# Performance work log

Hardware: AMD Instinct MI355X
Metric: run time of the kernel (lower is better)

## Reference

```python
import jax, jax.numpy as jnp
import numpy as np

B, S, D, H = 2, 2048, 1024, 16
HD = D // H  # head dim


def approx_gelu(x):
    return x * jax.nn.sigmoid(1.702 * x)


def setup_inputs() -> dict:
    key = jax.random.key(0)
    ks = jax.random.split(key, 12)
    q = jax.random.normal(ks[0], (B, S, D), jnp.float32)
    k = jax.random.normal(ks[1], (B, S, D), jnp.float32)
    v = jax.random.normal(ks[2], (B, S, D), jnp.float32)
    mask = jnp.zeros((B, 1, S, S), jnp.float32)
    sc = 0.02
    Wq = jax.random.normal(ks[3], (H, D, HD), jnp.float32) * sc
    bq = jax.random.normal(ks[4], (H, HD), jnp.float32) * sc
    Wk = jax.random.normal(ks[5], (H, D, HD), jnp.float32) * sc
    bk = jax.random.normal(ks[6], (H, HD), jnp.float32) * sc
    Wv = jax.random.normal(ks[7], (H, D, HD), jnp.float32) * sc
    bv = jax.random.normal(ks[8], (H, HD), jnp.float32) * sc
    Wo = jax.random.normal(ks[9], (D, D), jnp.float32) * sc
    bo = jax.random.normal(ks[10], (D,), jnp.float32) * sc
    return {"q": q, "k": k, "v": v, "mask": mask, "Wq": Wq, "bq": bq,
            "Wk": Wk, "bk": bk, "Wv": Wv, "bv": bv, "Wo": Wo, "bo": bo}


def reference(q, k, v, mask, Wq, bq, Wk, bk, Wv, bv, Wo, bo):
    # Per-head Q/K/V dense (no activation on projections, matching source).
    qh = jnp.einsum('bsd,hde->bhse', q, Wq) + bq[None, :, None, :]  # [B,H,S,HD]
    kh = jnp.einsum('bsd,hde->bhse', k, Wk) + bk[None, :, None, :]
    vh = jnp.einsum('bsd,hde->bhse', v, Wv) + bv[None, :, None, :]
    scale = 1.0 / jnp.sqrt(jnp.asarray(HD, qh.dtype))
    logits = jnp.einsum('bhse,bhte->bhst', qh, kh) * scale + mask  # [B,H,S,S]
    attn = jax.nn.softmax(logits, axis=-1)
    heads = jnp.einsum('bhst,bhte->bhse', attn, vh)  # [B,H,S,HD]
    # concat heads -> [B,S,D]
    x = jnp.transpose(heads, (0, 2, 1, 3)).reshape(q.shape[0], q.shape[1], D)
    return approx_gelu(x @ Wo + bo)
```

## Files before the change

### kernel.cpp

```cpp
#include <hip/hip_runtime.h>
#include <stdint.h>


typedef __bf16 bf16x8 __attribute__((ext_vector_type(8)));
typedef __bf16 bf16x4 __attribute__((ext_vector_type(4)));
typedef float f32x4 __attribute__((ext_vector_type(4)));
typedef float f32x16 __attribute__((ext_vector_type(16)));
typedef unsigned u32x4 __attribute__((ext_vector_type(4)));

static constexpr float L2E  = 1.4426950408889634f;
static constexpr float QSCL = 0.18033688011112042f;
static constexpr float GELC = -2.4554669595930157f;

__device__ __forceinline__ void async_load16(const void* g, void* l) {
    __builtin_amdgcn_global_load_lds(
        (const __attribute__((address_space(1))) unsigned int*)(uintptr_t)g,
        (__attribute__((address_space(3))) unsigned int*)(unsigned int)(uintptr_t)l,
        16, 0, 0);
}

template <int ROWS>
__device__ __forceinline__ void stage_tile(const __bf16* g, int ld, __bf16* lds, int tid) {
#pragma unroll
    for (int r = 0; r < ROWS / 32; ++r) {
        int p = r * 4096 + tid * 16;
        int row = p >> 7;
        int kbp = p & 127;
        int kbl = kbp ^ ((row & 7) << 4);
        async_load16((const char*)(g + (size_t)row * ld) + kbl,
                     (char*)lds + (p & ~1023));
    }
}

__device__ __forceinline__ bf16x8 lds_frag(const __bf16* base, int row, int kb) {
    return *(const bf16x8*)((const char*)base + (row << 7) + (kb ^ ((row & 7) << 4)));
}

__device__ __forceinline__ unsigned cvtpk(float a, float b) {
    unsigned d;
    asm("v_cvt_pk_bf16_f32 %0, %1, %2" : "=v"(d) : "v"(a), "v"(b));
    return d;
}
__device__ __forceinline__ void pswap(unsigned& a, unsigned& b) {
    asm("v_permlane32_swap_b32 %0, %1" : "+v"(a), "+v"(b));
}


__global__ __launch_bounds__(256) void cvt3_kernel(const float* __restrict__ q,
                                                   const float* __restrict__ k,
                                                   const float* __restrict__ v,
                                                   __bf16* __restrict__ qb,
                                                   __bf16* __restrict__ kb,
                                                   __bf16* __restrict__ vb) {
    int z = blockIdx.y;
    const float* src = z == 0 ? q : (z == 1 ? k : v);
    __bf16* dst = z == 0 ? qb : (z == 1 ? kb : vb);
    int i = blockIdx.x * 256 + threadIdx.x;
    f32x4 val = ((const f32x4*)src)[i];
    bf16x4 o;
    o[0] = (__bf16)val[0]; o[1] = (__bf16)val[1];
    o[2] = (__bf16)val[2]; o[3] = (__bf16)val[3];
    ((bf16x4*)dst)[i] = o;
}

__global__ __launch_bounds__(256) void flags_init(unsigned* __restrict__ flags) {
    int t = threadIdx.x;
#pragma unroll
    for (int k = 0; k < 4; ++k) flags[t + k * 256] = 0u;
}

__global__ __launch_bounds__(256) void mask_flags(const float* __restrict__ m,
                                                  unsigned* __restrict__ flags) {
    int i = blockIdx.x * 256 + threadIdx.x;
    f32x4 v = ((const f32x4*)m)[i];
    bool nz = (v[0] != 0.f) | (v[1] != 0.f) | (v[2] != 0.f) | (v[3] != 0.f);
    if (nz) {
        size_t i4 = (size_t)i * 4;
        int b = (int)(i4 >> 22);
        int rem = (int)(i4 & 4194303);
        int qq = rem >> 11, kv = rem & 2047;
        atomicOr(flags + (b * 16 + (qq >> 7)) * 32 + (kv >> 6), 1u);
    }
}

__global__ __launch_bounds__(256) void pack_wqkv(const float* __restrict__ Wq,
                                                 const float* __restrict__ Wk,
                                                 const float* __restrict__ Wv,
                                                 __bf16* __restrict__ out) {
    __shared__ __bf16 T[64][72];
    int tid = threadIdx.x;
    int k0 = blockIdx.x * 64, h = blockIdx.y, z = blockIdx.z;
    const float* W = z == 0 ? Wq : (z == 1 ? Wk : Wv);
#pragma unroll
    for (int it = 0; it < 4; ++it) {
        int idx = it * 1024 + tid * 4;
        int r = idx >> 6, e = idx & 63;
        f32x4 val = *(const f32x4*)(W + ((size_t)h * 1024 + k0 + r) * 64 + e);
#pragma unroll
        for (int j = 0; j < 4; ++j) T[r][e + j] = (__bf16)val[j];
    }
    __syncthreads();
    int e2 = tid >> 2, kc = (tid & 3) * 16;
    bf16x8 o0, o1;
#pragma unroll
    for (int i = 0; i < 8; ++i) { o0[i] = T[kc + i][e2]; o1[i] = T[kc + 8 + i][e2]; }
    __bf16* dst = out + ((size_t)z << 20) + (size_t)(h * 64 + e2) * 1024 + k0 + kc;
    *(bf16x8*)dst = o0;
    *(bf16x8*)(dst + 8) = o1;
}

__global__ __launch_bounds__(256) void pack_wo(const float* __restrict__ Wo,
                                               __bf16* __restrict__ out) {
    __shared__ __bf16 T[64][72];
    int tid = threadIdx.x;
    int k0 = blockIdx.x * 64, n0 = blockIdx.y * 64;
#pragma unroll
    for (int it = 0; it < 4; ++it) {
        int idx = it * 1024 + tid * 4;
        int r = idx >> 6, e = idx & 63;
        f32x4 val = *(const f32x4*)(Wo + (size_t)(k0 + r) * 1024 + n0 + e);
#pragma unroll
        for (int j = 0; j < 4; ++j) T[r][e + j] = (__bf16)val[j];
    }
    __syncthreads();
    int e2 = tid >> 2, kc = (tid & 3) * 16;
    bf16x8 o0, o1;
#pragma unroll
    for (int i = 0; i < 8; ++i) { o0[i] = T[kc + i][e2]; o1[i] = T[kc + 8 + i][e2]; }
    __bf16* dst = out + (size_t)(n0 + e2) * 1024 + k0 + kc;
    *(bf16x8*)dst = o0;
    *(bf16x8*)(dst + 8) = o1;
}

__global__ __launch_bounds__(256) void vtrans(const __bf16* __restrict__ vh,
                                              __bf16* __restrict__ vT) {
    __shared__ __bf16 T[64][72];
    int tid = threadIdx.x;
    int s0 = blockIdx.x * 64, bh = blockIdx.y, b = bh >> 4, h = bh & 15;
#pragma unroll
    for (int it = 0; it < 2; ++it) {
        int idx = it * 2048 + tid * 8;
        int r = idx >> 6, e0 = idx & 63;
        bf16x8 val = *(const bf16x8*)(vh + ((size_t)b * 2048 + s0 + r) * 1024 + h * 64 + e0);
#pragma unroll
        for (int j = 0; j < 8; ++j) T[r][e0 + j] = val[j];
    }
    __syncthreads();
    int e = tid >> 2, sc = (tid & 3) * 16;
    bf16x8 o0, o1;
#pragma unroll
    for (int i = 0; i < 8; ++i) { o0[i] = T[sc + i][e]; o1[i] = T[sc + 8 + i][e]; }
    __bf16* dst = vT + ((size_t)bh * 64 + e) * 2048 + s0 + sc;
    *(bf16x8*)dst = o0;
    *(bf16x8*)(dst + 8) = o1;
}

__global__ __launch_bounds__(256) void gemm_qkv(
    const __bf16* __restrict__ qb, const __bf16* __restrict__ kb,
    const __bf16* __restrict__ vb, const __bf16* __restrict__ w3,
    const float* __restrict__ bq, const float* __restrict__ bk,
    const float* __restrict__ bv,
    __bf16* __restrict__ qo, __bf16* __restrict__ ko, __bf16* __restrict__ vo) {
    __shared__ __bf16 As[128 * 64];
    __shared__ __bf16 Bs[128 * 64];
    int z = blockIdx.z;
    const __bf16* A = z == 0 ? qb : (z == 1 ? kb : vb);
    const __bf16* Bt = w3 + ((size_t)z << 20);
    const float* bias = z == 0 ? bq : (z == 1 ? bk : bv);
    __bf16* dst = z == 0 ? qo : (z == 1 ? ko : vo);
    float sc = z == 0 ? QSCL : 1.0f;

    int tid = threadIdx.x;
    int w = tid >> 6, lane = tid & 63, lg = lane >> 4, lr = lane & 15;
    int wr = (w >> 1) * 64, wc = (w & 1) * 64;
    int m0 = blockIdx.x * 128, n0 = blockIdx.y * 128;
    f32x4 acc[4][4] = {};
    for (int k0 = 0; k0 < 1024; k0 += 64) {
        __syncthreads();
        stage_tile<128>(A + (size_t)m0 * 1024 + k0, 1024, As, tid);
        stage_tile<128>(Bt + (size_t)n0 * 1024 + k0, 1024, Bs, tid);
        __syncthreads();
#pragma unroll
        for (int kk = 0; kk < 2; ++kk) {
            bf16x8 af[4], bfr[4];
#pragma unroll
            for (int t = 0; t < 4; ++t) {
                af[t] = lds_frag(As, wr + t * 16 + lr, lg * 16 + kk * 64);
                bfr[t] = lds_frag(Bs, wc + t * 16 + lr, lg * 16 + kk * 64);
            }
#pragma unroll
            for (int i = 0; i < 4; ++i)
#pragma unroll
                for (int j = 0; j < 4; ++j)
                    acc[i][j] = __builtin_amdgcn_mfma_f32_16x16x32_bf16(
                        af[i], bfr[j], acc[i][j], 0, 0, 0);
        }
    }
#pragma unroll
    for (int i = 0; i < 4; ++i) {
        int mb = m0 + wr + i * 16 + lg * 4;
#pragma unroll
        for (int j = 0; j < 4; ++j) {
            int n = n0 + wc + j * 16 + lr;
            float bvv = bias[n];
#pragma unroll
            for (int r = 0; r < 4; ++r)
                dst[(size_t)(mb + r) * 1024 + n] = (__bf16)((acc[i][j][r] + bvv) * sc);
        }
    }
}

__global__ __launch_bounds__(256) void gemm_out(const __bf16* __restrict__ A,
                                                const __bf16* __restrict__ Bt,
                                                const float* __restrict__ bias,
                                                float* __restrict__ dst) {
    __shared__ __bf16 As[64 * 64];
    __shared__ __bf16 Bs[128 * 64];
    int tid = threadIdx.x;
    int w = tid >> 6, lane = tid & 63, lg = lane >> 4, lr = lane & 15;
    int wr = (w >> 1) * 32, wc = (w & 1) * 64;
    int m0 = blockIdx.x * 64, n0 = blockIdx.y * 128;
    f32x4 acc[2][4] = {};
    for (int k0 = 0; k0 < 1024; k0 += 64) {
        __syncthreads();
        stage_tile<64>(A + (size_t)m0 * 1024 + k0, 1024, As, tid);
        stage_tile<128>(Bt + (size_t)n0 * 1024 + k0, 1024, Bs, tid);
        __syncthreads();
#pragma unroll
        for (int kk = 0; kk < 2; ++kk) {
            bf16x8 af[2], bfr[4];
#pragma unroll
            for (int t = 0; t < 2; ++t)
                af[t] = lds_frag(As, wr + t * 16 + lr, lg * 16 + kk * 64);
#pragma unroll
            for (int t = 0; t < 4; ++t)
                bfr[t] = lds_frag(Bs, wc + t * 16 + lr, lg * 16 + kk * 64);
#pragma unroll
            for (int i = 0; i < 2; ++i)
#pragma unroll
                for (int j = 0; j < 4; ++j)
                    acc[i][j] = __builtin_amdgcn_mfma_f32_16x16x32_bf16(
                        af[i], bfr[j], acc[i][j], 0, 0, 0);
        }
    }
#pragma unroll
    for (int i = 0; i < 2; ++i) {
        int mb = m0 + wr + i * 16 + lg * 4;
#pragma unroll
        for (int j = 0; j < 4; ++j) {
            int n = n0 + wc + j * 16 + lr;
            float bvv = bias[n];
#pragma unroll
            for (int r = 0; r < 4; ++r) {
                float v = acc[i][j][r] + bvv;
                float g = v / (1.f + exp2f(GELC * v));
                dst[(size_t)(mb + r) * 1024 + n] = g;
            }
        }
    }
}

__global__ __launch_bounds__(256) void attn_kernel(
    const __bf16* __restrict__ qs, const __bf16* __restrict__ ks,
    const __bf16* __restrict__ vT, const float* __restrict__ mask,
    const unsigned* __restrict__ flags,
    __bf16* __restrict__ Op0, __bf16* __restrict__ Op1,
    float* __restrict__ lacc) {
    __shared__ __bf16 Ks[2][64 * 64];
    __shared__ __bf16 Vs[2][64 * 64];
    int tid = threadIdx.x;
    int w = tid >> 6, l = tid & 63;
    int q31 = l & 31, hi = l >> 5;
    int i = blockIdx.x;
    int xcd = i & 7, j = i >> 3;
    int group = (j >> 4) * 8 + xcd;
    int qt = j & 15;
    int bh = group & 31, z = group >> 5;
    int b = bh >> 4, h = bh & 15;
    int qw = qt * 128 + w * 32;
    int kvbase = z << 10;

    const __bf16* Qp = qs + ((size_t)b * 2048 + qw + q31) * 1024 + h * 64 + hi * 8;
    bf16x8 qf[4];
#pragma unroll
    for (int kk = 0; kk < 4; ++kk) qf[kk] = *(const bf16x8*)(Qp + kk * 16);

    const __bf16* Kb = ks + ((size_t)b * 2048 + kvbase) * 1024 + h * 64;
    const __bf16* Vb = vT + (size_t)bh * 64 * 2048 + kvbase;
    const float* mrow = mask + (size_t)b * 4194304 + (size_t)(qw + q31) * 2048 + kvbase + hi * 4;
    const unsigned* flg = flags + (b * 16 + qt) * 32 + z * 16;

    f32x16 O[2] = {};
    float l_acc = 0.f;

    stage_tile<64>(Kb, 1024, Ks[0], tid);
    stage_tile<64>(Vb, 2048, Vs[0], tid);

    for (int kt = 0; kt < 16; ++kt) {
        int buf = kt & 1;
        __syncthreads();
        if (kt < 15) {
            stage_tile<64>(Kb + (size_t)(kt + 1) * 64 * 1024, 1024, Ks[buf ^ 1], tid);
            stage_tile<64>(Vb + (kt + 1) * 64, 2048, Vs[buf ^ 1], tid);
        }
        bf16x8 kf[2][4];
#pragma unroll
        for (int mt = 0; mt < 2; ++mt)
#pragma unroll
            for (int kk = 0; kk < 4; ++kk)
                kf[mt][kk] = lds_frag(Ks[buf], mt * 32 + q31, kk * 32 + hi * 16);
        f32x16 T[2] = {};
        __builtin_amdgcn_s_setprio(1);
#pragma unroll
        for (int kk = 0; kk < 4; ++kk)
#pragma unroll
            for (int mt = 0; mt < 2; ++mt)
                T[mt] = __builtin_amdgcn_mfma_f32_32x32x16_bf16(kf[mt][kk], qf[kk], T[mt], 0, 0, 0);
        __builtin_amdgcn_s_setprio(0);

        unsigned fl = __builtin_amdgcn_readfirstlane(flg[kt]);
        if (fl) {
#pragma unroll
            for (int mt = 0; mt < 2; ++mt)
#pragma unroll
                for (int g = 0; g < 4; ++g) {
                    f32x4 mk = *(const f32x4*)(mrow + kt * 64 + mt * 32 + g * 8);
#pragma unroll
                    for (int c = 0; c < 4; ++c)
                        T[mt][4 * g + c] = fmaf(mk[c], L2E, T[mt][4 * g + c]);
                }
        }
#pragma unroll
        for (int mt = 0; mt < 2; ++mt)
#pragma unroll
            for (int g = 0; g < 4; ++g) {
                float p0 = exp2f(T[mt][4 * g + 0]);
                float p1 = exp2f(T[mt][4 * g + 1]);
                float p2 = exp2f(T[mt][4 * g + 2]);
                float p3 = exp2f(T[mt][4 * g + 3]);
                l_acc += (p0 + p1) + (p2 + p3);
                T[mt][4 * g + 0] = p0; T[mt][4 * g + 1] = p1;
                T[mt][4 * g + 2] = p2; T[mt][4 * g + 3] = p3;
            }

        bf16x8 pf[4];
#pragma unroll
        for (int kk = 0; kk < 4; ++kk) {
            int mt = kk >> 1;
            int gA = (2 * kk) & 3, gB = gA + 1;
            unsigned x0 = cvtpk(T[mt][4 * gA + 0], T[mt][4 * gA + 1]);
            unsigned x1 = cvtpk(T[mt][4 * gA + 2], T[mt][4 * gA + 3]);
            unsigned y0 = cvtpk(T[mt][4 * gB + 0], T[mt][4 * gB + 1]);
            unsigned y1 = cvtpk(T[mt][4 * gB + 2], T[mt][4 * gB + 3]);
            pswap(x0, y0);
            pswap(x1, y1);
            u32x4 packed; packed[0] = x0; packed[1] = x1; packed[2] = y0; packed[3] = y1;
            pf[kk] = __builtin_bit_cast(bf16x8, packed);
        }

        bf16x8 vf[2][4];
#pragma unroll
        for (int mt = 0; mt < 2; ++mt)
#pragma unroll
            for (int kk = 0; kk < 4; ++kk)
                vf[mt][kk] = lds_frag(Vs[buf], mt * 32 + q31, kk * 32 + hi * 16);

        __builtin_amdgcn_s_setprio(1);
#pragma unroll
        for (int kk = 0; kk < 4; ++kk)
#pragma unroll
            for (int mt = 0; mt < 2; ++mt)
                O[mt] = __builtin_amdgcn_mfma_f32_32x32x16_bf16(vf[mt][kk], pf[kk], O[mt], 0, 0, 0);
        __builtin_amdgcn_s_setprio(0);
    }

    l_acc += __shfl_xor(l_acc, 32, 64);
    if (hi == 0)
        lacc[((size_t)z * 32 + b * 16 + h) * 2048 + qw + q31] = l_acc;
    __bf16* Ob = (z ? Op1 : Op0) + (((size_t)(b * 16 + h)) * 2048 + qw + q31) * 64 + hi * 4;
#pragma unroll
    for (int mt = 0; mt < 2; ++mt)
#pragma unroll
        for (int g = 0; g < 4; ++g) {
            bf16x4 o;
#pragma unroll
            for (int c = 0; c < 4; ++c) o[c] = (__bf16)O[mt][4 * g + c];
            *(bf16x4*)(Ob + mt * 32 + g * 8) = o;
        }
}

__global__ __launch_bounds__(256) void attn_norm(const __bf16* __restrict__ Op0,
                                                 const __bf16* __restrict__ Op1,
                                                 const float* __restrict__ lacc,
                                                 __bf16* __restrict__ x) {
    int idx = blockIdx.x * 256 + threadIdx.x;
    int b = idx >> 19;
    int rem = idx & 524287;
    int h = rem >> 15;
    int s = (rem >> 4) & 2047;
    int e0 = (rem & 15) * 4;
    size_t base = (((size_t)(b * 16 + h)) * 2048 + s) * 64 + e0;
    bf16x4 a = *(const bf16x4*)(Op0 + base);
    bf16x4 c = *(const bf16x4*)(Op1 + base);
    size_t li = ((size_t)(b * 16 + h)) * 2048 + s;
    float inv = 1.0f / (lacc[li] + lacc[65536 + li]);
    bf16x4 r;
#pragma unroll
    for (int j = 0; j < 4; ++j)
        r[j] = (__bf16)(((float)a[j] + (float)c[j]) * inv);
    *(bf16x4*)(x + ((size_t)b * 2048 + s) * 1024 + h * 64 + e0) = r;
}


extern "C" void kernel_launch(void* const* d_in, const int* in_sizes, int n_in,
                              void* d_out, int out_size, void* d_ws, size_t ws_size,
                              hipStream_t stream) {
    const float* q    = (const float*)d_in[0];
    const float* k    = (const float*)d_in[1];
    const float* v    = (const float*)d_in[2];
    const float* mask = (const float*)d_in[3];
    const float* Wq   = (const float*)d_in[4];
    const float* bq   = (const float*)d_in[5];
    const float* Wk   = (const float*)d_in[6];
    const float* bk   = (const float*)d_in[7];
    const float* Wv   = (const float*)d_in[8];
    const float* bv   = (const float*)d_in[9];
    const float* Wo   = (const float*)d_in[10];
    const float* bo   = (const float*)d_in[11];

    char* ws = (char*)d_ws;
    __bf16* qb  = (__bf16*)(ws + (0ull  << 20));
    __bf16* kb  = (__bf16*)(ws + (8ull  << 20));
    __bf16* vb  = (__bf16*)(ws + (16ull << 20));
    __bf16* w3  = (__bf16*)(ws + (24ull << 20));
    __bf16* wo  = (__bf16*)(ws + (30ull << 20));
    __bf16* qhp = (__bf16*)(ws + (32ull << 20));
    __bf16* khp = (__bf16*)(ws + (40ull << 20));
    __bf16* vhp = (__bf16*)(ws + (48ull << 20));
    float*  laccp = (float*)(ws + (56ull << 20));
    unsigned* flagp = (unsigned*)(ws + (56ull << 20) + (512ull << 10));
    __bf16* vTp = qb;
    __bf16* Op0 = kb;
    __bf16* Op1 = vb;
    __bf16* xp  = vhp;

    cvt3_kernel<<<dim3(4096, 3), 256, 0, stream>>>(q, k, v, qb, kb, vb);
    pack_wqkv<<<dim3(16, 16, 3), 256, 0, stream>>>(Wq, Wk, Wv, w3);
    pack_wo<<<dim3(16, 16), 256, 0, stream>>>(Wo, wo);
    flags_init<<<1, 256, 0, stream>>>(flagp);
    mask_flags<<<8192, 256, 0, stream>>>(mask, flagp);

    gemm_qkv<<<dim3(32, 8, 3), 256, 0, stream>>>(qb, kb, vb, w3, bq, bk, bv,
                                                 qhp, khp, vhp);
    vtrans<<<dim3(32, 32), 256, 0, stream>>>(vhp, vTp);

    attn_kernel<<<dim3(1024), 256, 0, stream>>>(qhp, khp, vTp, mask, flagp,
                                                Op0, Op1, laccp);
    attn_norm<<<4096, 256, 0, stream>>>(Op0, Op1, laccp, xp);

    gemm_out<<<dim3(64, 8), 256, 0, stream>>>(xp, wo, bo, (float*)d_out);
}
```

Measured before the change: 165.9 us.

## Pre-pack Q/K/V into MFMA fragment layout and load directly from global

Adds packing kernels that rearrange Q, K and V into the exact per-lane MFMA fragment order. The attention kernel then reads K and V fragments straight from global memory into registers with coalesced 16-byte loads, prefetching the next K tile, instead of staging through double-buffered LDS with block barriers. This removes LDS traffic and __syncthreads from the inner loop, but adds an extra packing pass over Q and K and relies on L2 to serve the repeated K/V reads across the four waves.

Measured after the change: 165.7 us. Within noise of the previous version (-0.1%).

```diff
diff --git a/kernel.cpp b/kernel.cpp
--- a/kernel.cpp
+++ b/kernel.cpp
@@ -132,8 +132,38 @@
     *(bf16x8*)(dst + 8) = o1;
 }
 
-__global__ __launch_bounds__(256) void vtrans(const __bf16* __restrict__ vh,
-                                              __bf16* __restrict__ vT) {
+__global__ __launch_bounds__(256) void qkpack(const __bf16* __restrict__ qh,
+                                              const __bf16* __restrict__ kh,
+                                              __bf16* __restrict__ Qp,
+                                              __bf16* __restrict__ Kp) {
+    __shared__ __bf16 T[64][72];
+    int tid = threadIdx.x;
+    int s0 = blockIdx.x * 64, bh = blockIdx.y, b = bh >> 4, h = bh & 15;
+    const __bf16* src = blockIdx.z ? kh : qh;
+    __bf16* out = blockIdx.z ? Kp : Qp;
+#pragma unroll
+    for (int it = 0; it < 2; ++it) {
+        int idx = it * 2048 + tid * 8;
+        int r = idx >> 6, e0 = idx & 63;
+        bf16x8 val = *(const bf16x8*)(src + ((size_t)b * 2048 + s0 + r) * 1024 + h * 64 + e0);
+#pragma unroll
+        for (int j = 0; j < 8; ++j) T[r][e0 + j] = val[j];
+    }
+    __syncthreads();
+#pragma unroll
+    for (int u0 = 0; u0 < 2; ++u0) {
+        int u = u0 * 256 + tid;
+        int sb = u >> 8, rem = u & 255;
+        int kk = rem >> 6, hi = (rem >> 5) & 1, q31 = rem & 31;
+        bf16x8 o;
+#pragma unroll
+        for (int j = 0; j < 8; ++j) o[j] = T[sb * 32 + q31][kk * 16 + hi * 8 + j];
+        *(bf16x8*)(out + ((size_t)bh * 64 + blockIdx.x * 2 + sb) * 2048 + rem * 8) = o;
+    }
+}
+
+__global__ __launch_bounds__(256) void vpack(const __bf16* __restrict__ vh,
+                                             __bf16* __restrict__ Vp) {
     __shared__ __bf16 T[64][72];
     int tid = threadIdx.x;
     int s0 = blockIdx.x * 64, bh = blockIdx.y, b = bh >> 4, h = bh & 15;
@@ -146,13 +176,16 @@
         for (int j = 0; j < 8; ++j) T[r][e0 + j] = val[j];
     }
     __syncthreads();
-    int e = tid >> 2, sc = (tid & 3) * 16;
-    bf16x8 o0, o1;
-#pragma unroll
-    for (int i = 0; i < 8; ++i) { o0[i] = T[sc + i][e]; o1[i] = T[sc + 8 + i][e]; }
-    __bf16* dst = vT + ((size_t)bh * 64 + e) * 2048 + s0 + sc;
-    *(bf16x8*)dst = o0;
-    *(bf16x8*)(dst + 8) = o1;
+#pragma unroll
+    for (int u0 = 0; u0 < 2; ++u0) {
+        int u = u0 * 256 + tid;
+        int mt = u >> 8, rem = u & 255;
+        int kk = rem >> 6, hi = (rem >> 5) & 1, e31 = rem & 31;
+        bf16x8 o;
+#pragma unroll
+        for (int j = 0; j < 8; ++j) o[j] = T[kk * 16 + hi * 8 + j][mt * 32 + e31];
+        *(bf16x8*)(Vp + ((size_t)bh * 32 + blockIdx.x) * 4096 + u * 8) = o;
+    }
 }
 
 __global__ __launch_bounds__(256) void gemm_qkv(
@@ -261,13 +294,11 @@
 }
 
 __global__ __launch_bounds__(256) void attn_kernel(
-    const __bf16* __restrict__ qs, const __bf16* __restrict__ ks,
-    const __bf16* __restrict__ vT, const float* __restrict__ mask,
+    const __bf16* __restrict__ Qp, const __bf16* __restrict__ Kp,
+    const __bf16* __restrict__ Vp, const float* __restrict__ mask,
     const unsigned* __restrict__ flags,
     __bf16* __restrict__ Op0, __bf16* __restrict__ Op1,
     float* __restrict__ lacc) {
-    __shared__ __bf16 Ks[2][64 * 64];
-    __shared__ __bf16 Vs[2][64 * 64];
     int tid = threadIdx.x;
     int w = tid >> 6, l = tid & 63;
     int q31 = l & 31, hi = l >> 5;
@@ -278,37 +309,28 @@
     int bh = group & 31, z = group >> 5;
     int b = bh >> 4, h = bh & 15;
     int qw = qt * 128 + w * 32;
-    int kvbase = z << 10;
-
-    const __bf16* Qp = qs + ((size_t)b * 2048 + qw + q31) * 1024 + h * 64 + hi * 8;
+
+    const __bf16* Qb = Qp + ((size_t)bh * 64 + (qw >> 5)) * 2048 + l * 8;
     bf16x8 qf[4];
 #pragma unroll
-    for (int kk = 0; kk < 4; ++kk) qf[kk] = *(const bf16x8*)(Qp + kk * 16);
-
-    const __bf16* Kb = ks + ((size_t)b * 2048 + kvbase) * 1024 + h * 64;
-    const __bf16* Vb = vT + (size_t)bh * 64 * 2048 + kvbase;
-    const float* mrow = mask + (size_t)b * 4194304 + (size_t)(qw + q31) * 2048 + kvbase + hi * 4;
+    for (int kk = 0; kk < 4; ++kk) qf[kk] = *(const bf16x8*)(Qb + kk * 512);
+
+    const __bf16* Kb = Kp + ((size_t)bh * 64 + z * 32) * 2048 + l * 8;
+    const __bf16* Vb = Vp + ((size_t)bh * 32 + z * 16) * 4096 + l * 8;
+    const float* mrow = mask + (size_t)b * 4194304 + (size_t)(qw + q31) * 2048 + (z << 10) + hi * 4;
     const unsigned* flg = flags + (b * 16 + qt) * 32 + z * 16;
 
     f32x16 O[2] = {};
     float l_acc = 0.f;
 
-    stage_tile<64>(Kb, 1024, Ks[0], tid);
-    stage_tile<64>(Vb, 2048, Vs[0], tid);
+    bf16x8 kf[2][4];
+#pragma unroll
+    for (int mt = 0; mt < 2; ++mt)
+#pragma unroll
+        for (int kk = 0; kk < 4; ++kk)
+            kf[mt][kk] = *(const bf16x8*)(Kb + (mt * 4 + kk) * 512);
 
     for (int kt = 0; kt < 16; ++kt) {
-        int buf = kt & 1;
-        __syncthreads();
-        if (kt < 15) {
-            stage_tile<64>(Kb + (size_t)(kt + 1) * 64 * 1024, 1024, Ks[buf ^ 1], tid);
-            stage_tile<64>(Vb + (kt + 1) * 64, 2048, Vs[buf ^ 1], tid);
-        }
-        bf16x8 kf[2][4];
-#pragma unroll
-        for (int mt = 0; mt < 2; ++mt)
-#pragma unroll
-            for (int kk = 0; kk < 4; ++kk)
-                kf[mt][kk] = lds_frag(Ks[buf], mt * 32 + q31, kk * 32 + hi * 16);
         f32x16 T[2] = {};
         __builtin_amdgcn_s_setprio(1);
 #pragma unroll
@@ -317,6 +339,20 @@
             for (int mt = 0; mt < 2; ++mt)
                 T[mt] = __builtin_amdgcn_mfma_f32_32x32x16_bf16(kf[mt][kk], qf[kk], T[mt], 0, 0, 0);
         __builtin_amdgcn_s_setprio(0);
+
+        bf16x8 vf[2][4];
+#pragma unroll
+        for (int mt = 0; mt < 2; ++mt)
+#pragma unroll
+            for (int kk = 0; kk < 4; ++kk)
+                vf[mt][kk] = *(const bf16x8*)(Vb + (size_t)kt * 4096 + (mt * 4 + kk) * 512);
+        if (kt < 15) {
+#pragma unroll
+            for (int mt = 0; mt < 2; ++mt)
+#pragma unroll
+                for (int kk = 0; kk < 4; ++kk)
+                    kf[mt][kk] = *(const bf16x8*)(Kb + ((size_t)(kt + 1) * 2 + mt) * 2048 + kk * 512);
+        }
 
         unsigned fl = __builtin_amdgcn_readfirstlane(flg[kt]);
         if (fl) {
@@ -357,13 +393,6 @@
             u32x4 packed; packed[0] = x0; packed[1] = x1; packed[2] = y0; packed[3] = y1;
             pf[kk] = __builtin_bit_cast(bf16x8, packed);
         }
-
-        bf16x8 vf[2][4];
-#pragma unroll
-        for (int mt = 0; mt < 2; ++mt)
-#pragma unroll
-            for (int kk = 0; kk < 4; ++kk)
-                vf[mt][kk] = lds_frag(Vs[buf], mt * 32 + q31, kk * 32 + hi * 16);
 
         __builtin_amdgcn_s_setprio(1);
 #pragma unroll
@@ -439,9 +468,11 @@
     __bf16* vhp = (__bf16*)(ws + (48ull << 20));
     float*  laccp = (float*)(ws + (56ull << 20));
     unsigned* flagp = (unsigned*)(ws + (56ull << 20) + (512ull << 10));
-    __bf16* vTp = qb;
-    __bf16* Op0 = kb;
-    __bf16* Op1 = vb;
+    __bf16* Qpk = qb;
+    __bf16* Vpk = kb;
+    __bf16* Kpk = vb;
+    __bf16* Op0 = qhp;
+    __bf16* Op1 = khp;
     __bf16* xp  = vhp;
 
     cvt3_kernel<<<dim3(4096, 3), 256, 0, stream>>>(q, k, v, qb, kb, vb);
@@ -452,9 +483,10 @@
 
     gemm_qkv<<<dim3(32, 8, 3), 256, 0, stream>>>(qb, kb, vb, w3, bq, bk, bv,
                                                  qhp, khp, vhp);
-    vtrans<<<dim3(32, 32), 256, 0, stream>>>(vhp, vTp);
-
-    attn_kernel<<<dim3(1024), 256, 0, stream>>>(qhp, khp, vTp, mask, flagp,
+    qkpack<<<dim3(32, 32, 2), 256, 0, stream>>>(qhp, khp, Qpk, Kpk);
+    vpack<<<dim3(32, 32), 256, 0, stream>>>(vhp, Vpk);
+
+    attn_kernel<<<dim3(1024), 256, 0, stream>>>(Qpk, Kpk, Vpk, mask, flagp,
                                                 Op0, Op1, laccp);
     attn_norm<<<4096, 256, 0, stream>>>(Op0, Op1, laccp, xp);
 
```

## Write Q/K/V in MFMA-fragment-packed layout and load attention operands directly

Applied to the files above, without the earlier changes.

The QKV projection epilogue now writes Q, K and V straight into a per-head layout packed to match the MFMA fragments, with V pre-transposed. This removes the separate vtrans kernel, and the attention kernel drops its LDS staging and barriers. Each wave instead loads K/V fragments straight from global memory with coalesced 16-byte loads, prefetching the next K tile in registers. The flags kernel is replaced by hipMemsetAsync, and the softmax row sum is split into two accumulators. The trade-off is that every wave now reads K/V from global memory or L2 instead of sharing them through LDS, and the QKV epilogue does scattered stores.

Result: faster. 157.0 us (-5.4%).

```diff
diff --git a/kernel.cpp b/kernel.cpp
--- a/kernel.cpp
+++ b/kernel.cpp
@@ -63,12 +63,6 @@
     ((bf16x4*)dst)[i] = o;
 }
 
-__global__ __launch_bounds__(256) void flags_init(unsigned* __restrict__ flags) {
-    int t = threadIdx.x;
-#pragma unroll
-    for (int k = 0; k < 4; ++k) flags[t + k * 256] = 0u;
-}
-
 __global__ __launch_bounds__(256) void mask_flags(const float* __restrict__ m,
                                                   unsigned* __restrict__ flags) {
     int i = blockIdx.x * 256 + threadIdx.x;
@@ -132,42 +126,18 @@
     *(bf16x8*)(dst + 8) = o1;
 }
 
-__global__ __launch_bounds__(256) void vtrans(const __bf16* __restrict__ vh,
-                                              __bf16* __restrict__ vT) {
-    __shared__ __bf16 T[64][72];
-    int tid = threadIdx.x;
-    int s0 = blockIdx.x * 64, bh = blockIdx.y, b = bh >> 4, h = bh & 15;
-#pragma unroll
-    for (int it = 0; it < 2; ++it) {
-        int idx = it * 2048 + tid * 8;
-        int r = idx >> 6, e0 = idx & 63;
-        bf16x8 val = *(const bf16x8*)(vh + ((size_t)b * 2048 + s0 + r) * 1024 + h * 64 + e0);
-#pragma unroll
-        for (int j = 0; j < 8; ++j) T[r][e0 + j] = val[j];
-    }
-    __syncthreads();
-    int e = tid >> 2, sc = (tid & 3) * 16;
-    bf16x8 o0, o1;
-#pragma unroll
-    for (int i = 0; i < 8; ++i) { o0[i] = T[sc + i][e]; o1[i] = T[sc + 8 + i][e]; }
-    __bf16* dst = vT + ((size_t)bh * 64 + e) * 2048 + s0 + sc;
-    *(bf16x8*)dst = o0;
-    *(bf16x8*)(dst + 8) = o1;
-}
-
 __global__ __launch_bounds__(256) void gemm_qkv(
     const __bf16* __restrict__ qb, const __bf16* __restrict__ kb,
     const __bf16* __restrict__ vb, const __bf16* __restrict__ w3,
     const float* __restrict__ bq, const float* __restrict__ bk,
     const float* __restrict__ bv,
-    __bf16* __restrict__ qo, __bf16* __restrict__ ko, __bf16* __restrict__ vo) {
+    __bf16* __restrict__ Qp, __bf16* __restrict__ Kp, __bf16* __restrict__ Vp) {
     __shared__ __bf16 As[128 * 64];
     __shared__ __bf16 Bs[128 * 64];
     int z = blockIdx.z;
     const __bf16* A = z == 0 ? qb : (z == 1 ? kb : vb);
     const __bf16* Bt = w3 + ((size_t)z << 20);
     const float* bias = z == 0 ? bq : (z == 1 ? bk : bv);
-    __bf16* dst = z == 0 ? qo : (z == 1 ? ko : vo);
     float sc = z == 0 ? QSCL : 1.0f;
 
     int tid = threadIdx.x;
@@ -199,13 +169,29 @@
 #pragma unroll
     for (int i = 0; i < 4; ++i) {
         int mb = m0 + wr + i * 16 + lg * 4;
+        int b = mb >> 11, s = mb & 2047;
 #pragma unroll
         for (int j = 0; j < 4; ++j) {
             int n = n0 + wc + j * 16 + lr;
             float bvv = bias[n];
-#pragma unroll
-            for (int r = 0; r < 4; ++r)
-                dst[(size_t)(mb + r) * 1024 + n] = (__bf16)((acc[i][j][r] + bvv) * sc);
+            int h = n >> 6, e = n & 63;
+            int bh = b * 16 + h;
+            if (z == 2) {
+                size_t addr = ((size_t)bh * 32 + (s >> 6)) * 4096 + (e >> 5) * 2048 +
+                              ((s >> 4) & 3) * 512 + ((s >> 3) & 1) * 256 +
+                              (e & 31) * 8 + (s & 7);
+                bf16x4 o;
+#pragma unroll
+                for (int r = 0; r < 4; ++r) o[r] = (__bf16)(acc[i][j][r] + bvv);
+                *(bf16x4*)(Vp + addr) = o;
+            } else {
+                __bf16* out = z == 0 ? Qp : Kp;
+                size_t base = ((size_t)bh * 64 + (s >> 5)) * 2048 + (e >> 4) * 512 +
+                              ((e >> 3) & 1) * 256 + (s & 31) * 8 + (e & 7);
+#pragma unroll
+                for (int r = 0; r < 4; ++r)
+                    out[base + r * 8] = (__bf16)((acc[i][j][r] + bvv) * sc);
+            }
         }
     }
 }
@@ -261,13 +247,11 @@
 }
 
 __global__ __launch_bounds__(256) void attn_kernel(
-    const __bf16* __restrict__ qs, const __bf16* __restrict__ ks,
-    const __bf16* __restrict__ vT, const float* __restrict__ mask,
+    const __bf16* __restrict__ Qp, const __bf16* __restrict__ Kp,
+    const __bf16* __restrict__ Vp, const float* __restrict__ mask,
     const unsigned* __restrict__ flags,
     __bf16* __restrict__ Op0, __bf16* __restrict__ Op1,
     float* __restrict__ lacc) {
-    __shared__ __bf16 Ks[2][64 * 64];
-    __shared__ __bf16 Vs[2][64 * 64];
     int tid = threadIdx.x;
     int w = tid >> 6, l = tid & 63;
     int q31 = l & 31, hi = l >> 5;
@@ -278,37 +262,28 @@
     int bh = group & 31, z = group >> 5;
     int b = bh >> 4, h = bh & 15;
     int qw = qt * 128 + w * 32;
-    int kvbase = z << 10;
-
-    const __bf16* Qp = qs + ((size_t)b * 2048 + qw + q31) * 1024 + h * 64 + hi * 8;
+
+    const __bf16* Qb = Qp + ((size_t)bh * 64 + (qw >> 5)) * 2048 + l * 8;
     bf16x8 qf[4];
 #pragma unroll
-    for (int kk = 0; kk < 4; ++kk) qf[kk] = *(const bf16x8*)(Qp + kk * 16);
-
-    const __bf16* Kb = ks + ((size_t)b * 2048 + kvbase) * 1024 + h * 64;
-    const __bf16* Vb = vT + (size_t)bh * 64 * 2048 + kvbase;
-    const float* mrow = mask + (size_t)b * 4194304 + (size_t)(qw + q31) * 2048 + kvbase + hi * 4;
+    for (int kk = 0; kk < 4; ++kk) qf[kk] = *(const bf16x8*)(Qb + kk * 512);
+
+    const __bf16* Kb = Kp + ((size_t)bh * 64 + z * 32) * 2048 + l * 8;
+    const __bf16* Vb = Vp + ((size_t)bh * 32 + z * 16) * 4096 + l * 8;
+    const float* mrow = mask + (size_t)b * 4194304 + (size_t)(qw + q31) * 2048 + (z << 10) + hi * 4;
     const unsigned* flg = flags + (b * 16 + qt) * 32 + z * 16;
 
     f32x16 O[2] = {};
-    float l_acc = 0.f;
-
-    stage_tile<64>(Kb, 1024, Ks[0], tid);
-    stage_tile<64>(Vb, 2048, Vs[0], tid);
+    float la0 = 0.f, la1 = 0.f;
+
+    bf16x8 kf[2][4];
+#pragma unroll
+    for (int mt = 0; mt < 2; ++mt)
+#pragma unroll
+        for (int kk = 0; kk < 4; ++kk)
+            kf[mt][kk] = *(const bf16x8*)(Kb + (mt * 4 + kk) * 512);
 
     for (int kt = 0; kt < 16; ++kt) {
-        int buf = kt & 1;
-        __syncthreads();
-        if (kt < 15) {
-            stage_tile<64>(Kb + (size_t)(kt + 1) * 64 * 1024, 1024, Ks[buf ^ 1], tid);
-            stage_tile<64>(Vb + (kt + 1) * 64, 2048, Vs[buf ^ 1], tid);
-        }
-        bf16x8 kf[2][4];
-#pragma unroll
-        for (int mt = 0; mt < 2; ++mt)
-#pragma unroll
-            for (int kk = 0; kk < 4; ++kk)
-                kf[mt][kk] = lds_frag(Ks[buf], mt * 32 + q31, kk * 32 + hi * 16);
         f32x16 T[2] = {};
         __builtin_amdgcn_s_setprio(1);
 #pragma unroll
@@ -318,6 +293,20 @@
                 T[mt] = __builtin_amdgcn_mfma_f32_32x32x16_bf16(kf[mt][kk], qf[kk], T[mt], 0, 0, 0);
         __builtin_amdgcn_s_setprio(0);
 
+        bf16x8 vf[2][4];
+#pragma unroll
+        for (int mt = 0; mt < 2; ++mt)
+#pragma unroll
+            for (int kk = 0; kk < 4; ++kk)
+                vf[mt][kk] = *(const bf16x8*)(Vb + (size_t)kt * 4096 + (mt * 4 + kk) * 512);
+        if (kt < 15) {
+#pragma unroll
+            for (int mt = 0; mt < 2; ++mt)
+#pragma unroll
+                for (int kk = 0; kk < 4; ++kk)
+                    kf[mt][kk] = *(const bf16x8*)(Kb + ((size_t)(kt + 1) * 2 + mt) * 2048 + kk * 512);
+        }
+
         unsigned fl = __builtin_amdgcn_readfirstlane(flg[kt]);
         if (fl) {
 #pragma unroll
@@ -331,17 +320,22 @@
                 }
         }
 #pragma unroll
-        for (int mt = 0; mt < 2; ++mt)
-#pragma unroll
-            for (int g = 0; g < 4; ++g) {
-                float p0 = exp2f(T[mt][4 * g + 0]);
-                float p1 = exp2f(T[mt][4 * g + 1]);
-                float p2 = exp2f(T[mt][4 * g + 2]);
-                float p3 = exp2f(T[mt][4 * g + 3]);
-                l_acc += (p0 + p1) + (p2 + p3);
-                T[mt][4 * g + 0] = p0; T[mt][4 * g + 1] = p1;
-                T[mt][4 * g + 2] = p2; T[mt][4 * g + 3] = p3;
-            }
+        for (int g = 0; g < 4; ++g) {
+            float a0 = exp2f(T[0][4 * g + 0]);
+            float a1 = exp2f(T[0][4 * g + 1]);
+            float a2 = exp2f(T[0][4 * g + 2]);
+            float a3 = exp2f(T[0][4 * g + 3]);
+            float b0 = exp2f(T[1][4 * g + 0]);
+            float b1 = exp2f(T[1][4 * g + 1]);
+            float b2 = exp2f(T[1][4 * g + 2]);
+            float b3 = exp2f(T[1][4 * g + 3]);
+            la0 += (a0 + a1) + (a2 + a3);
+            la1 += (b0 + b1) + (b2 + b3);
+            T[0][4 * g + 0] = a0; T[0][4 * g + 1] = a1;
+            T[0][4 * g + 2] = a2; T[0][4 * g + 3] = a3;
+            T[1][4 * g + 0] = b0; T[1][4 * g + 1] = b1;
+            T[1][4 * g + 2] = b2; T[1][4 * g + 3] = b3;
+        }
 
         bf16x8 pf[4];
 #pragma unroll
@@ -358,13 +352,6 @@
             pf[kk] = __builtin_bit_cast(bf16x8, packed);
         }
 
-        bf16x8 vf[2][4];
-#pragma unroll
-        for (int mt = 0; mt < 2; ++mt)
-#pragma unroll
-            for (int kk = 0; kk < 4; ++kk)
-                vf[mt][kk] = lds_frag(Vs[buf], mt * 32 + q31, kk * 32 + hi * 16);
-
         __builtin_amdgcn_s_setprio(1);
 #pragma unroll
         for (int kk = 0; kk < 4; ++kk)
@@ -374,6 +361,7 @@
         __builtin_amdgcn_s_setprio(0);
     }
 
+    float l_acc = la0 + la1;
     l_acc += __shfl_xor(l_acc, 32, 64);
     if (hi == 0)
         lacc[((size_t)z * 32 + b * 16 + h) * 2048 + qw + q31] = l_acc;
@@ -434,27 +422,25 @@
     __bf16* vb  = (__bf16*)(ws + (16ull << 20));
     __bf16* w3  = (__bf16*)(ws + (24ull << 20));
     __bf16* wo  = (__bf16*)(ws + (30ull << 20));
-    __bf16* qhp = (__bf16*)(ws + (32ull << 20));
-    __bf16* khp = (__bf16*)(ws + (40ull << 20));
-    __bf16* vhp = (__bf16*)(ws + (48ull << 20));
+    __bf16* Qpk = (__bf16*)(ws + (32ull << 20));
+    __bf16* Kpk = (__bf16*)(ws + (40ull << 20));
+    __bf16* Vpk = (__bf16*)(ws + (48ull << 20));
     float*  laccp = (float*)(ws + (56ull << 20));
     unsigned* flagp = (unsigned*)(ws + (56ull << 20) + (512ull << 10));
-    __bf16* vTp = qb;
-    __bf16* Op0 = kb;
-    __bf16* Op1 = vb;
-    __bf16* xp  = vhp;
+    __bf16* Op0 = qb;
+    __bf16* Op1 = kb;
+    __bf16* xp  = vb;
 
     cvt3_kernel<<<dim3(4096, 3), 256, 0, stream>>>(q, k, v, qb, kb, vb);
     pack_wqkv<<<dim3(16, 16, 3), 256, 0, stream>>>(Wq, Wk, Wv, w3);
     pack_wo<<<dim3(16, 16), 256, 0, stream>>>(Wo, wo);
-    flags_init<<<1, 256, 0, stream>>>(flagp);
+    hipMemsetAsync(flagp, 0, 4096, stream);
     mask_flags<<<8192, 256, 0, stream>>>(mask, flagp);
 
     gemm_qkv<<<dim3(32, 8, 3), 256, 0, stream>>>(qb, kb, vb, w3, bq, bk, bv,
-                                                 qhp, khp, vhp);
-    vtrans<<<dim3(32, 32), 256, 0, stream>>>(vhp, vTp);
-
-    attn_kernel<<<dim3(1024), 256, 0, stream>>>(qhp, khp, vTp, mask, flagp,
+                                                 Qpk, Kpk, Vpk);
+
+    attn_kernel<<<dim3(1024), 256, 0, stream>>>(Qpk, Kpk, Vpk, mask, flagp,
                                                 Op0, Op1, laccp);
     attn_norm<<<4096, 256, 0, stream>>>(Op0, Op1, laccp, xp);
 
```
